# Optimization experiments

Hardware: AMD Instinct MI355X
Metric: run time of the kernel (lower is better)

## Reference

```python
import jax, jax.numpy as jnp
import numpy as np

NUM_NODES = 32768  # B*N = 16*2048
NUM_REL = 10
NUM_BASES = 4
D = 256
E = 524288


def _rgcn_layer(x, src, dst, rel, basis, comp, root, bias):
    """Basis-decomposed relational GCN layer with per-relation mean aggregation.
    x: [N, Din], basis: [NB, Din, Dout], comp: [R, NB], root: [Din, Dout], bias: [Dout].
    """
    n = x.shape[0]
    # project all nodes through each basis once: [N, NB, Dout]
    xb = jnp.einsum('ni,bio->nbo', x, basis)
    coeff = comp[rel]  # [E, NB] per-edge basis coefficients
    # mean normalization per (destination node, relation) pair
    seg = rel * n + dst  # combined segment id, [E]
    cnt = jax.ops.segment_sum(jnp.ones(rel.shape[0], x.dtype), seg,
                              num_segments=NUM_REL * n)
    inv = jnp.where(cnt > 0, 1.0 / cnt, 0.0)[seg]  # [E]
    # per-edge message: sum_b coeff[e,b] * xb[src_e, b, :] (loop over small NB)
    msg = jnp.zeros((rel.shape[0], basis.shape[2]), x.dtype)
    for b in range(basis.shape[0]):
        msg = msg + coeff[:, b:b + 1] * xb[src, b]
    msg = msg * inv[:, None]
    agg = jax.ops.segment_sum(msg, dst, num_segments=n)  # [N, Dout]
    return agg + x @ root + bias


def setup_inputs() -> dict:
    key = jax.random.key(0)
    ks = jax.random.split(key, 16)
    p = lambda k, shp: (jax.random.normal(k, shp, jnp.float32) * 0.05)
    inp = {
        'x': jax.random.normal(ks[0], (16, 2048, D), jnp.float32),
        't': jax.random.randint(ks[1], (16,), 0, 1000),
        'obj_cond': jax.random.randint(ks[2], (16, 2048), 0, 160),
        'edge_cond': jax.random.randint(ks[3], (2, E), 0, NUM_NODES),
        'relation_cond': jax.random.randint(ks[4], (E,), 0, NUM_REL),
        # layer 0: 256 -> 256 (hidden)
        'basis0': p(ks[5], (NUM_BASES, D, D)),
        'comp0': p(ks[6], (NUM_REL, NUM_BASES)),
        'root0': p(ks[7], (D, D)),
        'bias0': p(ks[8], (D,)),
        # layer 1: 256 -> 256 (output)
        'basis1': p(ks[9], (NUM_BASES, D, D)),
        'comp1': p(ks[10], (NUM_REL, NUM_BASES)),
        'root1': p(ks[11], (D, D)),
        'bias1': p(ks[12], (D,)),
    }
    return inp


def reference(x, t, obj_cond, edge_cond, relation_cond,
              basis0, comp0, root0, bias0, basis1, comp1, root1, bias1):
    B, N, Dm = x.shape
    h = x.reshape(B * N, Dm)
    src, dst = edge_cond[0], edge_cond[1]
    h = _rgcn_layer(h, src, dst, relation_cond, basis0, comp0, root0, bias0)
    h = jax.nn.relu(h)  # hidden-layer activation (dropout disabled at eval)
    h = _rgcn_layer(h, src, dst, relation_cond, basis1, comp1, root1, bias1)
    return h.reshape(B, N, Dm)
```

## Files before the change

kernel.cpp:

```cpp
#include <hip/hip_runtime.h>
#include <stdint.h>

#define NNODES 32768
#define NREL 10
#define NBASES 4
#define DIM 256
#define NEDGE 524288
#define KW 1280
#define KBASE 1024

typedef __attribute__((ext_vector_type(8))) short bf16x8;
typedef __attribute__((ext_vector_type(4))) float f32x4;

__device__ __forceinline__ float bf2f(unsigned short u){
  union { unsigned int i; float f; } v; v.i = ((unsigned int)u) << 16; return v.f;
}
__device__ __forceinline__ unsigned short f2bf(float f){
  union { float f; unsigned int i; } v; v.f = f;
  unsigned int x = v.i;
  unsigned int r = (x + 0x7FFFu + ((x >> 16) & 1u)) >> 16;
  return (unsigned short)r;
}
__device__ __forceinline__ void gll16(const void* g, void* l){
  __builtin_amdgcn_global_load_lds((const __attribute__((address_space(1))) void*)g,
                                   (__attribute__((address_space(3))) void*)l, 16, 0, 0);
}

__global__ __launch_bounds__(256) void conv_kernel(const float* __restrict__ in,
                                                   unsigned short* __restrict__ out)
{
  int i = blockIdx.x * 256 + threadIdx.x;
  float4 v = ((const float4*)in)[i];
  ushort4 o; o.x = f2bf(v.x); o.y = f2bf(v.y); o.z = f2bf(v.z); o.w = f2bf(v.w);
  ((ushort4*)out)[i] = o;
}

__global__ void hist_kernel(const int* __restrict__ ec, const int* __restrict__ rel,
                            int* __restrict__ cnt_rd)
{
  int e = blockIdx.x * 256 + threadIdx.x;
  int d = ec[NEDGE + e];
  int r = rel[e];
  atomicAdd(&cnt_rd[(r << 15) + d], 1);
}

__global__ __launch_bounds__(1024) void scan1(const int* __restrict__ cnt_rd,
                                              int* __restrict__ offs, int* __restrict__ blksum)
{
  __shared__ int sh[1024];
  int tid = threadIdx.x; int gid = blockIdx.x * 1024 + tid;
  int v = 0;
#pragma unroll
  for (int r = 0; r < NREL; r++) v += cnt_rd[(r << 15) + gid];
  sh[tid] = v; __syncthreads();
  for (int off = 1; off < 1024; off <<= 1){
    int t = (tid >= off) ? sh[tid - off] : 0;
    __syncthreads(); sh[tid] += t; __syncthreads();
  }
  offs[gid] = sh[tid] - v;
  if (tid == 1023) blksum[blockIdx.x] = sh[1023];
}
__global__ __launch_bounds__(64) void scan2(int* __restrict__ blksum)
{
  __shared__ int sh[64];
  int tid = threadIdx.x;
  int v = (tid < NNODES / 1024) ? blksum[tid] : 0;
  sh[tid] = v; __syncthreads();
  for (int off = 1; off < 64; off <<= 1){
    int t = (tid >= off) ? sh[tid - off] : 0;
    __syncthreads(); sh[tid] += t; __syncthreads();
  }
  if (tid < NNODES / 1024) blksum[tid] = sh[tid] - v;
}
__global__ __launch_bounds__(1024) void scan3(int* __restrict__ offs, const int* __restrict__ blksum)
{
  int gid = blockIdx.x * 1024 + threadIdx.x;
  offs[gid] += blksum[blockIdx.x];
  if (gid == 0) offs[NNODES] = NEDGE;
}

__global__ void scatter_kernel(const int* __restrict__ ec, const int* __restrict__ rel,
                               const int* __restrict__ offs, int* __restrict__ cursor,
                               const int* __restrict__ cnt_rd,
                               uint2* __restrict__ meta)
{
  int e = blockIdx.x * 256 + threadIdx.x;
  int s = ec[e];
  int d = ec[NEDGE + e];
  int r = rel[e];
  int p = offs[d] + atomicAdd(&cursor[d], 1);
  float inv = 1.0f / (float)cnt_rd[(r << 15) + d];
  uint2 m; m.x = ((unsigned int)s << 4) | (unsigned int)r;
  m.y = __float_as_uint(inv);
  meta[p] = m;
}

__global__ __launch_bounds__(256) void build_wt3(
    const float* __restrict__ basis,
    const float* __restrict__ root,
    unsigned short* __restrict__ Wt)
{
  __shared__ float tile[64][65];
  int t = threadIdx.x;
  int k0 = blockIdx.x * 64;
  int n0 = blockIdx.y * 64;
  int tn = t & 63, tk = t >> 6;
#pragma unroll
  for (int i = 0; i < 64; i += 4){
    int k = k0 + tk + i;
    float v = (k < KBASE) ? basis[(size_t)k * 256 + n0 + tn]
                          : root[(size_t)(k - KBASE) * 256 + n0 + tn];
    tile[tk + i][tn] = v;
  }
  __syncthreads();
#pragma unroll
  for (int i = 0; i < 64; i += 4){
    int n = n0 + tk + i;
    Wt[(size_t)n * KW + k0 + tn] = f2bf(tile[tn][tk + i]);
  }
}

__global__ __launch_bounds__(256) void agg4(
    const unsigned short* __restrict__ Xin,
    const int* __restrict__ offs,
    const uint2* __restrict__ meta,
    const float* __restrict__ comp,
    unsigned short* __restrict__ z)
{
  __shared__ float scomp[NREL * NBASES];
  int t = threadIdx.x;
  if (t < NREL * NBASES) scomp[t] = comp[t];
  __syncthreads();
  int d = blockIdx.x * 4 + (t >> 6);
  int col = (t & 63) * 4;

  float acc[NBASES][4] = {};
  int e0 = offs[d], e1 = offs[d + 1];
  int e = e0;
  for (; e + 3 < e1; e += 4){
    uint2 m0 = meta[e], m1 = meta[e + 1], m2 = meta[e + 2], m3 = meta[e + 3];
    ushort4 v0 = *(const ushort4*)(Xin + ((size_t)(m0.x >> 4)) * 256 + col);
    ushort4 v1 = *(const ushort4*)(Xin + ((size_t)(m1.x >> 4)) * 256 + col);
    ushort4 v2 = *(const ushort4*)(Xin + ((size_t)(m2.x >> 4)) * 256 + col);
    ushort4 v3 = *(const ushort4*)(Xin + ((size_t)(m3.x >> 4)) * 256 + col);
#pragma unroll
    for (int b = 0; b < NBASES; b++){
      float w0 = __uint_as_float(m0.y) * scomp[(m0.x & 15u) * NBASES + b];
      float w1 = __uint_as_float(m1.y) * scomp[(m1.x & 15u) * NBASES + b];
      float w2 = __uint_as_float(m2.y) * scomp[(m2.x & 15u) * NBASES + b];
      float w3 = __uint_as_float(m3.y) * scomp[(m3.x & 15u) * NBASES + b];
      acc[b][0] += w0 * bf2f(v0.x) + w1 * bf2f(v1.x) + w2 * bf2f(v2.x) + w3 * bf2f(v3.x);
      acc[b][1] += w0 * bf2f(v0.y) + w1 * bf2f(v1.y) + w2 * bf2f(v2.y) + w3 * bf2f(v3.y);
      acc[b][2] += w0 * bf2f(v0.z) + w1 * bf2f(v1.z) + w2 * bf2f(v2.z) + w3 * bf2f(v3.z);
      acc[b][3] += w0 * bf2f(v0.w) + w1 * bf2f(v1.w) + w2 * bf2f(v2.w) + w3 * bf2f(v3.w);
    }
  }
  for (; e < e1; ++e){
    uint2 md = meta[e];
    int s = (int)(md.x >> 4);
    float inv = __uint_as_float(md.y);
    ushort4 v = *(const ushort4*)(Xin + (size_t)s * 256 + col);
    const float* c = scomp + (md.x & 15u) * NBASES;
#pragma unroll
    for (int b = 0; b < NBASES; b++){
      float w = inv * c[b];
      acc[b][0] += w * bf2f(v.x); acc[b][1] += w * bf2f(v.y);
      acc[b][2] += w * bf2f(v.z); acc[b][3] += w * bf2f(v.w);
    }
  }
#pragma unroll
  for (int b = 0; b < NBASES; b++){
    ushort4 o;
    o.x = f2bf(acc[b][0]); o.y = f2bf(acc[b][1]);
    o.z = f2bf(acc[b][2]); o.w = f2bf(acc[b][3]);
    *(ushort4*)(z + (size_t)d * KBASE + b * 256 + col) = o;
  }
}

__global__ __launch_bounds__(256) void gemm4(
    const unsigned short* __restrict__ A0,
    const unsigned short* __restrict__ A1,
    const unsigned short* __restrict__ Wt,
    const float* __restrict__ bias,
    unsigned short* __restrict__ outh,
    float* __restrict__ outf,
    int mode)
{
  __shared__ __attribute__((aligned(16))) short As[64 * 32];
  __shared__ __attribute__((aligned(16))) short Bs[256 * 32];
  int tid  = threadIdx.x;
  int m0   = blockIdx.x * 64;
  int lane = tid & 63;
  int wn   = tid >> 6;
  int lq = lane >> 4, lr = lane & 15;

  f32x4 zero = {0.f, 0.f, 0.f, 0.f};
  f32x4 acc[4][4];
#pragma unroll
  for (int i = 0; i < 4; i++)
#pragma unroll
    for (int j = 0; j < 4; j++) acc[i][j] = zero;

  int arow = tid >> 2;
  int akc  = ((tid & 3) - (tid >> 3)) & 3;

  for (int k0 = 0; k0 < KW; k0 += 32){
    __syncthreads();
    {
      const unsigned short* ga;
      if (k0 < KBASE) ga = A0 + (size_t)(m0 + arow) * KBASE + k0 + akc * 8;
      else            ga = A1 + (size_t)(m0 + arow) * 256 + (k0 - KBASE) + akc * 8;
      gll16(ga, As + tid * 8);
    }
#pragma unroll
    for (int i = 0; i < 4; i++){
      int gb  = tid + i * 256;
      int row = gb >> 2;
      int kc  = ((gb & 3) - (gb >> 3)) & 3;
      gll16(Wt + (size_t)row * KW + k0 + kc * 8, Bs + gb * 8);
    }
    __syncthreads();

    bf16x8 af[4], bfr[4];
#pragma unroll
    for (int i = 0; i < 4; i++){
      int row = i * 16 + lr;
      af[i] = *(const bf16x8*)(As + row * 32 + (((lq + (row >> 1)) & 3) * 8));
    }
#pragma unroll
    for (int j = 0; j < 4; j++){
      int row = wn * 64 + j * 16 + lr;
      bfr[j] = *(const bf16x8*)(Bs + row * 32 + (((lq + (row >> 1)) & 3) * 8));
    }
#pragma unroll
    for (int i = 0; i < 4; i++)
#pragma unroll
      for (int j = 0; j < 4; j++)
        acc[i][j] = __builtin_amdgcn_mfma_f32_16x16x32_bf16(af[i], bfr[j], acc[i][j], 0, 0, 0);
  }

#pragma unroll
  for (int i = 0; i < 4; i++)
#pragma unroll
    for (int j = 0; j < 4; j++)
#pragma unroll
      for (int r = 0; r < 4; r++){
        int gm = m0 + i * 16 + lq * 4 + r;
        int gn = wn * 64 + j * 16 + lr;
        float v = acc[i][j][r] + bias[gn];
        size_t idx = (size_t)gm * 256 + gn;
        if (mode == 1) outh[idx] = f2bf(fmaxf(v, 0.f));
        else           outf[idx] = v;
      }
}

extern "C" void kernel_launch(void* const* d_in, const int* in_sizes, int n_in,
                              void* d_out, int out_size, void* d_ws, size_t ws_size,
                              hipStream_t stream)
{
  const float* x      = (const float*)d_in[0];
  const int*   ec     = (const int*)d_in[3];
  const int*   rel    = (const int*)d_in[4];
  const float* basis0 = (const float*)d_in[5];
  const float* comp0  = (const float*)d_in[6];
  const float* root0  = (const float*)d_in[7];
  const float* bias0  = (const float*)d_in[8];
  const float* basis1 = (const float*)d_in[9];
  const float* comp1  = (const float*)d_in[10];
  const float* root1  = (const float*)d_in[11];
  const float* bias1  = (const float*)d_in[12];

  char* p = (char*)d_ws;
  unsigned short* z  = (unsigned short*)p; p += (size_t)NNODES * KBASE * 2;
  unsigned short* Xh = (unsigned short*)p; p += (size_t)NNODES * DIM * 2;
  unsigned short* h  = (unsigned short*)p; p += (size_t)NNODES * DIM * 2;
  unsigned short* Wt = (unsigned short*)p; p += (size_t)256 * KW * 2;
  uint2* meta  = (uint2*)p; p += (size_t)NEDGE * 8;
  int* cnt_rd  = (int*)p;   p += (size_t)NREL * NNODES * 4;
  int* cursor  = (int*)p;   p += (size_t)NNODES * 4;
  int* offs    = (int*)p;   p += (size_t)(NNODES + 1) * 4;
  int* blksum  = (int*)p;   p += 1024;

  hipMemsetAsync(cnt_rd, 0, ((size_t)NREL * NNODES + (size_t)NNODES) * 4, stream);

  hist_kernel   <<<NEDGE / 256, 256, 0, stream>>>(ec, rel, cnt_rd);
  scan1         <<<NNODES / 1024, 1024, 0, stream>>>(cnt_rd, offs, blksum);
  scan2         <<<1, 64, 0, stream>>>(blksum);
  scan3         <<<NNODES / 1024, 1024, 0, stream>>>(offs, blksum);
  scatter_kernel<<<NEDGE / 256, 256, 0, stream>>>(ec, rel, offs, cursor, cnt_rd, meta);

  conv_kernel<<<(NNODES * DIM / 4) / 256, 256, 0, stream>>>(x, Xh);

  dim3 wgrid(KW / 64, 256 / 64);

  build_wt3<<<wgrid, 256, 0, stream>>>(basis0, root0, Wt);
  agg4<<<NNODES / 4, 256, 0, stream>>>(Xh, offs, meta, comp0, z);
  gemm4<<<NNODES / 64, 256, 0, stream>>>(z, Xh, Wt, bias0, h, nullptr, 1);

  build_wt3<<<wgrid, 256, 0, stream>>>(basis1, root1, Wt);
  agg4<<<NNODES / 4, 256, 0, stream>>>(h, offs, meta, comp1, z);
  gemm4<<<NNODES / 64, 256, 0, stream>>>(z, h, Wt, bias1, nullptr, (float*)d_out, 2);
}
```

Before: 333.0 us.

## Shrink edge metadata and precompute per-node relation weights; enlarge GEMM M tile

Edge metadata is packed into a single 32-bit word (source and relation), and the mean normalisation is moved out of it. Each aggregation wave now builds a per-destination table of comp[r,b]/cnt in LDS and reads one float4 per edge. This halves the metadata traffic and removes per-edge multiplies. The GEMM tile grows from 64 to 128 rows so each B tile load is reused across twice as many rows, at the cost of more accumulator registers and half as many blocks.

```diff
diff --git a/kernel.cpp b/kernel.cpp
--- a/kernel.cpp
+++ b/kernel.cpp
@@ -81,18 +81,14 @@
 
 __global__ void scatter_kernel(const int* __restrict__ ec, const int* __restrict__ rel,
                                const int* __restrict__ offs, int* __restrict__ cursor,
-                               const int* __restrict__ cnt_rd,
-                               uint2* __restrict__ meta)
+                               unsigned int* __restrict__ meta)
 {
   int e = blockIdx.x * 256 + threadIdx.x;
   int s = ec[e];
   int d = ec[NEDGE + e];
   int r = rel[e];
   int p = offs[d] + atomicAdd(&cursor[d], 1);
-  float inv = 1.0f / (float)cnt_rd[(r << 15) + d];
-  uint2 m; m.x = ((unsigned int)s << 4) | (unsigned int)r;
-  m.y = __float_as_uint(inv);
-  meta[p] = m;
+  meta[p] = ((unsigned int)s << 4) | (unsigned int)r;
 }
 
 __global__ __launch_bounds__(256) void build_wt3(
@@ -120,52 +116,59 @@
   }
 }
 
-__global__ __launch_bounds__(256) void agg4(
+__global__ __launch_bounds__(256) void agg5(
     const unsigned short* __restrict__ Xin,
     const int* __restrict__ offs,
-    const uint2* __restrict__ meta,
+    const unsigned int* __restrict__ meta,
     const float* __restrict__ comp,
+    const int* __restrict__ cnt_rd,
     unsigned short* __restrict__ z)
 {
-  __shared__ float scomp[NREL * NBASES];
+  __shared__ __attribute__((aligned(16))) float wtab[4][40];
   int t = threadIdx.x;
-  if (t < NREL * NBASES) scomp[t] = comp[t];
+  int wv = t >> 6, lane = t & 63;
+  int d = blockIdx.x * 4 + wv;
+  if (lane < 40){
+    int r = lane >> 2, b = lane & 3;
+    int cnt = cnt_rd[(r << 15) + d];
+    wtab[wv][lane] = (cnt > 0) ? comp[r * NBASES + b] / (float)cnt : 0.0f;
+  }
   __syncthreads();
-  int d = blockIdx.x * 4 + (t >> 6);
-  int col = (t & 63) * 4;
+
+  int col = lane * 4;
+  const float4* wt4 = (const float4*)&wtab[wv][0];
 
   float acc[NBASES][4] = {};
   int e0 = offs[d], e1 = offs[d + 1];
   int e = e0;
   for (; e + 3 < e1; e += 4){
-    uint2 m0 = meta[e], m1 = meta[e + 1], m2 = meta[e + 2], m3 = meta[e + 3];
-    ushort4 v0 = *(const ushort4*)(Xin + ((size_t)(m0.x >> 4)) * 256 + col);
-    ushort4 v1 = *(const ushort4*)(Xin + ((size_t)(m1.x >> 4)) * 256 + col);
-    ushort4 v2 = *(const ushort4*)(Xin + ((size_t)(m2.x >> 4)) * 256 + col);
-    ushort4 v3 = *(const ushort4*)(Xin + ((size_t)(m3.x >> 4)) * 256 + col);
+    unsigned int m0 = meta[e], m1 = meta[e + 1], m2 = meta[e + 2], m3 = meta[e + 3];
+    float4 w0 = wt4[m0 & 15u], w1 = wt4[m1 & 15u], w2 = wt4[m2 & 15u], w3 = wt4[m3 & 15u];
+    ushort4 v0 = *(const ushort4*)(Xin + ((size_t)(m0 >> 4)) * 256 + col);
+    ushort4 v1 = *(const ushort4*)(Xin + ((size_t)(m1 >> 4)) * 256 + col);
+    ushort4 v2 = *(const ushort4*)(Xin + ((size_t)(m2 >> 4)) * 256 + col);
+    ushort4 v3 = *(const ushort4*)(Xin + ((size_t)(m3 >> 4)) * 256 + col);
 #pragma unroll
     for (int b = 0; b < NBASES; b++){
-      float w0 = __uint_as_float(m0.y) * scomp[(m0.x & 15u) * NBASES + b];
-      float w1 = __uint_as_float(m1.y) * scomp[(m1.x & 15u) * NBASES + b];
-      float w2 = __uint_as_float(m2.y) * scomp[(m2.x & 15u) * NBASES + b];
-      float w3 = __uint_as_float(m3.y) * scomp[(m3.x & 15u) * NBASES + b];
-      acc[b][0] += w0 * bf2f(v0.x) + w1 * bf2f(v1.x) + w2 * bf2f(v2.x) + w3 * bf2f(v3.x);
-      acc[b][1] += w0 * bf2f(v0.y) + w1 * bf2f(v1.y) + w2 * bf2f(v2.y) + w3 * bf2f(v3.y);
-      acc[b][2] += w0 * bf2f(v0.z) + w1 * bf2f(v1.z) + w2 * bf2f(v2.z) + w3 * bf2f(v3.z);
-      acc[b][3] += w0 * bf2f(v0.w) + w1 * bf2f(v1.w) + w2 * bf2f(v2.w) + w3 * bf2f(v3.w);
+      float a0 = ((const float*)&w0)[b];
+      float a1 = ((const float*)&w1)[b];
+      float a2 = ((const float*)&w2)[b];
+      float a3 = ((const float*)&w3)[b];
+      acc[b][0] += a0 * bf2f(v0.x) + a1 * bf2f(v1.x) + a2 * bf2f(v2.x) + a3 * bf2f(v3.x);
+      acc[b][1] += a0 * bf2f(v0.y) + a1 * bf2f(v1.y) + a2 * bf2f(v2.y) + a3 * bf2f(v3.y);
+      acc[b][2] += a0 * bf2f(v0.z) + a1 * bf2f(v1.z) + a2 * bf2f(v2.z) + a3 * bf2f(v3.z);
+      acc[b][3] += a0 * bf2f(v0.w) + a1 * bf2f(v1.w) + a2 * bf2f(v2.w) + a3 * bf2f(v3.w);
     }
   }
   for (; e < e1; ++e){
-    uint2 md = meta[e];
-    int s = (int)(md.x >> 4);
-    float inv = __uint_as_float(md.y);
-    ushort4 v = *(const ushort4*)(Xin + (size_t)s * 256 + col);
-    const float* c = scomp + (md.x & 15u) * NBASES;
+    unsigned int md = meta[e];
+    float4 w = wt4[md & 15u];
+    ushort4 v = *(const ushort4*)(Xin + ((size_t)(md >> 4)) * 256 + col);
 #pragma unroll
     for (int b = 0; b < NBASES; b++){
-      float w = inv * c[b];
-      acc[b][0] += w * bf2f(v.x); acc[b][1] += w * bf2f(v.y);
-      acc[b][2] += w * bf2f(v.z); acc[b][3] += w * bf2f(v.w);
+      float a = ((const float*)&w)[b];
+      acc[b][0] += a * bf2f(v.x); acc[b][1] += a * bf2f(v.y);
+      acc[b][2] += a * bf2f(v.z); acc[b][3] += a * bf2f(v.w);
     }
   }
 #pragma unroll
@@ -177,7 +180,7 @@
   }
 }
 
-__global__ __launch_bounds__(256) void gemm4(
+__global__ __launch_bounds__(256) void gemm5(
     const unsigned short* __restrict__ A0,
     const unsigned short* __restrict__ A1,
     const unsigned short* __restrict__ Wt,
@@ -186,44 +189,45 @@
     float* __restrict__ outf,
     int mode)
 {
-  __shared__ __attribute__((aligned(16))) short As[64 * 32];
+  __shared__ __attribute__((aligned(16))) short As[128 * 32];
   __shared__ __attribute__((aligned(16))) short Bs[256 * 32];
   int tid  = threadIdx.x;
-  int m0   = blockIdx.x * 64;
+  int m0   = blockIdx.x * 128;
   int lane = tid & 63;
   int wn   = tid >> 6;
   int lq = lane >> 4, lr = lane & 15;
 
   f32x4 zero = {0.f, 0.f, 0.f, 0.f};
-  f32x4 acc[4][4];
-#pragma unroll
-  for (int i = 0; i < 4; i++)
+  f32x4 acc[8][4];
+#pragma unroll
+  for (int i = 0; i < 8; i++)
 #pragma unroll
     for (int j = 0; j < 4; j++) acc[i][j] = zero;
-
-  int arow = tid >> 2;
-  int akc  = ((tid & 3) - (tid >> 3)) & 3;
 
   for (int k0 = 0; k0 < KW; k0 += 32){
     __syncthreads();
-    {
+#pragma unroll
+    for (int i = 0; i < 2; i++){
+      int g   = tid + i * 256;
+      int row = g >> 2;
+      int kc  = ((g & 3) - (g >> 3)) & 3;
       const unsigned short* ga;
-      if (k0 < KBASE) ga = A0 + (size_t)(m0 + arow) * KBASE + k0 + akc * 8;
-      else            ga = A1 + (size_t)(m0 + arow) * 256 + (k0 - KBASE) + akc * 8;
-      gll16(ga, As + tid * 8);
+      if (k0 < KBASE) ga = A0 + (size_t)(m0 + row) * KBASE + k0 + kc * 8;
+      else            ga = A1 + (size_t)(m0 + row) * 256 + (k0 - KBASE) + kc * 8;
+      gll16(ga, As + g * 8);
     }
 #pragma unroll
     for (int i = 0; i < 4; i++){
-      int gb  = tid + i * 256;
-      int row = gb >> 2;
-      int kc  = ((gb & 3) - (gb >> 3)) & 3;
-      gll16(Wt + (size_t)row * KW + k0 + kc * 8, Bs + gb * 8);
+      int g   = tid + i * 256;
+      int row = g >> 2;
+      int kc  = ((g & 3) - (g >> 3)) & 3;
+      gll16(Wt + (size_t)row * KW + k0 + kc * 8, Bs + g * 8);
     }
     __syncthreads();
 
-    bf16x8 af[4], bfr[4];
-#pragma unroll
-    for (int i = 0; i < 4; i++){
+    bf16x8 af[8], bfr[4];
+#pragma unroll
+    for (int i = 0; i < 8; i++){
       int row = i * 16 + lr;
       af[i] = *(const bf16x8*)(As + row * 32 + (((lq + (row >> 1)) & 3) * 8));
     }
@@ -233,14 +237,14 @@
       bfr[j] = *(const bf16x8*)(Bs + row * 32 + (((lq + (row >> 1)) & 3) * 8));
     }
 #pragma unroll
-    for (int i = 0; i < 4; i++)
+    for (int i = 0; i < 8; i++)
 #pragma unroll
       for (int j = 0; j < 4; j++)
         acc[i][j] = __builtin_amdgcn_mfma_f32_16x16x32_bf16(af[i], bfr[j], acc[i][j], 0, 0, 0);
   }
 
 #pragma unroll
-  for (int i = 0; i < 4; i++)
+  for (int i = 0; i < 8; i++)
 #pragma unroll
     for (int j = 0; j < 4; j++)
 #pragma unroll
@@ -275,7 +279,7 @@
   unsigned short* Xh = (unsigned short*)p; p += (size_t)NNODES * DIM * 2;
   unsigned short* h  = (unsigned short*)p; p += (size_t)NNODES * DIM * 2;
   unsigned short* Wt = (unsigned short*)p; p += (size_t)256 * KW * 2;
-  uint2* meta  = (uint2*)p; p += (size_t)NEDGE * 8;
+  unsigned int* meta = (unsigned int*)p; p += (size_t)NEDGE * 4;
   int* cnt_rd  = (int*)p;   p += (size_t)NREL * NNODES * 4;
   int* cursor  = (int*)p;   p += (size_t)NNODES * 4;
   int* offs    = (int*)p;   p += (size_t)(NNODES + 1) * 4;
@@ -287,17 +291,17 @@
   scan1         <<<NNODES / 1024, 1024, 0, stream>>>(cnt_rd, offs, blksum);
   scan2         <<<1, 64, 0, stream>>>(blksum);
   scan3         <<<NNODES / 1024, 1024, 0, stream>>>(offs, blksum);
-  scatter_kernel<<<NEDGE / 256, 256, 0, stream>>>(ec, rel, offs, cursor, cnt_rd, meta);
+  scatter_kernel<<<NEDGE / 256, 256, 0, stream>>>(ec, rel, offs, cursor, meta);
 
   conv_kernel<<<(NNODES * DIM / 4) / 256, 256, 0, stream>>>(x, Xh);
 
   dim3 wgrid(KW / 64, 256 / 64);
 
   build_wt3<<<wgrid, 256, 0, stream>>>(basis0, root0, Wt);
-  agg4<<<NNODES / 4, 256, 0, stream>>>(Xh, offs, meta, comp0, z);
-  gemm4<<<NNODES / 64, 256, 0, stream>>>(z, Xh, Wt, bias0, h, nullptr, 1);
+  agg5<<<NNODES / 4, 256, 0, stream>>>(Xh, offs, meta, comp0, cnt_rd, z);
+  gemm5<<<NNODES / 128, 256, 0, stream>>>(z, Xh, Wt, bias0, h, nullptr, 1);
 
   build_wt3<<<wgrid, 256, 0, stream>>>(basis1, root1, Wt);
-  agg4<<<NNODES / 4, 256, 0, stream>>>(h, offs, meta, comp1, z);
-  gemm4<<<NNODES / 64, 256, 0, stream>>>(z, h, Wt, bias1, nullptr, (float*)d_out, 2);
-}
+  agg5<<<NNODES / 4, 256, 0, stream>>>(h, offs, meta, comp1, cnt_rd, z);
+  gemm5<<<NNODES / 128, 256, 0, stream>>>(z, h, Wt, bias1, nullptr, (float*)d_out, 2);
+}
```

After: 381.6 us. 14.6% more time.
